# Performance work log

Hardware: AMD Instinct MI355X
Metric: run time of the kernel (lower is better)

The kernel has to match this reference:

```python
import jax, jax.numpy as jnp
import numpy as np

N = 50000   # nodes
E = 800000  # edges
IN = 64     # in_channels
ED = 16     # edge_dim
H = 4       # heads
C = 64      # per-head out channels (gnn_hidden_neurons)
G = 2048    # number of graphs in batch
OUT = 1
SLOPE = 0.2


def setup_inputs() -> dict:
    key = jax.random.key(0)
    ks = jax.random.split(key, 20)
    s = lambda fan_in: 1.0 / np.sqrt(fan_in)
    inp = {
        "x": jax.random.normal(ks[0], (N, IN), dtype=jnp.float32),
        "edge_index": jax.random.randint(ks[1], (2, E), 0, N, dtype=jnp.int64),
        "batch": jnp.sort(jax.random.randint(ks[2], (N,), 0, G, dtype=jnp.int64)),
        "edge_attr": jax.random.normal(ks[3], (E, ED), dtype=jnp.float32),
        # GATv2Conv layer 1 (in=IN)
        "Wl1": jax.random.normal(ks[4], (IN, H * C), dtype=jnp.float32) * s(IN),
        "Wr1": jax.random.normal(ks[5], (IN, H * C), dtype=jnp.float32) * s(IN),
        "We1": jax.random.normal(ks[6], (ED, H * C), dtype=jnp.float32) * s(ED),
        "att1": jax.random.normal(ks[7], (H, C), dtype=jnp.float32) * s(C),
        "b1": jnp.zeros((H * C,), dtype=jnp.float32),
        # GATv2Conv layer 2 (in=H*C)
        "Wl2": jax.random.normal(ks[8], (H * C, H * C), dtype=jnp.float32) * s(H * C),
        "Wr2": jax.random.normal(ks[9], (H * C, H * C), dtype=jnp.float32) * s(H * C),
        "We2": jax.random.normal(ks[10], (ED, H * C), dtype=jnp.float32) * s(ED),
        "att2": jax.random.normal(ks[11], (H, C), dtype=jnp.float32) * s(C),
        "b2": jnp.zeros((H * C,), dtype=jnp.float32),
        # FFN: Linear(H*C, OUT)
        "Wf": jax.random.normal(ks[12], (H * C, OUT), dtype=jnp.float32) * s(H * C),
        "bf": jnp.zeros((OUT,), dtype=jnp.float32),
    }
    return inp


def gatv2_layer(x, src, dst, ea, Wl, Wr, We, att, b):
    # x: [N, F], src/dst: [E2], ea: [E2, ED] (self-loops already included)
    n = x.shape[0]
    e2 = src.shape[0]
    xl = (x @ Wl).reshape(n, H, C)          # source transform
    xr = (x @ Wr).reshape(n, H, C)          # target transform
    ee = (ea @ We).reshape(e2, H, C)        # edge transform
    e = xl[src] + xr[dst] + ee              # [E2, H, C]
    e = jnp.where(e > 0, e, SLOPE * e)      # leaky_relu(0.2)
    score = jnp.einsum('ehc,hc->eh', e, att)
    # segment softmax over incoming edges of each destination node
    m = jax.ops.segment_max(score, dst, num_segments=n)
    m = jnp.where(jnp.isfinite(m), m, 0.0)
    ex = jnp.exp(score - m[dst])
    denom = jax.ops.segment_sum(ex, dst, num_segments=n)
    alpha = ex / (denom[dst] + 1e-16)       # [E2, H]
    out = jax.ops.segment_sum(alpha[:, :, None] * xl[src], dst, num_segments=n)
    return out.reshape(n, H * C) + b


def reference(x, edge_index, batch, edge_attr,
              Wl1, Wr1, We1, att1, b1,
              Wl2, Wr2, We2, att2, b2,
              Wf, bf):
    src, dst = edge_index[0], edge_index[1]
    # add self loops with fill_value='mean' edge attr (PyG GATv2Conv default)
    loop = jnp.arange(N, dtype=src.dtype)
    src2 = jnp.concatenate([src, loop])
    dst2 = jnp.concatenate([dst, loop])
    mean_ea = jnp.mean(edge_attr, axis=0)
    ea2 = jnp.concatenate([edge_attr, jnp.broadcast_to(mean_ea, (N, ED))], axis=0)

    h = gatv2_layer(x, src2, dst2, ea2, Wl1, Wr1, We1, att1, b1)
    h = jax.nn.relu(h)                      # activation (dropout = identity at eval)
    h = gatv2_layer(h, src2, dst2, ea2, Wl2, Wr2, We2, att2, b2)
    h = jax.nn.relu(h)

    # global mean pooling over graphs
    counts = jax.ops.segment_sum(jnp.ones((N,), dtype=h.dtype), batch, num_segments=G)
    pooled = jax.ops.segment_sum(h, batch, num_segments=G) / jnp.maximum(counts, 1.0)[:, None]

    # ffn_nlayers == 1: Dropout (identity) + Linear
    return pooled @ Wf + bf
```

## Files before the change

kernel.cpp:

```cpp
#include <hip/hip_runtime.h>
#include <math.h>

#define NN 50000
#define NE 800000
#define NE2 (NE + NN)
#define INC 64
#define EDD 16
#define NH 4
#define CC 64
#define HC 256
#define NG 2048
#define SLOPE 0.2f

typedef float v2f __attribute__((ext_vector_type(2)));
typedef float v4f __attribute__((ext_vector_type(4)));

#define RFL(x) __builtin_amdgcn_readfirstlane(x)

template <int CTRL, int RM>
__device__ __forceinline__ float dpp_add(float x) {
  int t = __builtin_amdgcn_update_dpp(0, __builtin_bit_cast(int, x),
                                      CTRL, RM, 0xF, false);
  return x + __builtin_bit_cast(float, t);
}
__device__ __forceinline__ float wave_sum_bcast(float x) {
  x = dpp_add<0x111, 0xF>(x);
  x = dpp_add<0x112, 0xF>(x);
  x = dpp_add<0x114, 0xF>(x);
  x = dpp_add<0x118, 0xF>(x);
  x = dpp_add<0x142, 0xA>(x);
  x = dpp_add<0x143, 0xC>(x);
  return __builtin_bit_cast(float,
      __builtin_amdgcn_readlane(__builtin_bit_cast(int, x), 63));
}

__global__ void ea_sum_kernel(const float* __restrict__ ea, float* __restrict__ meansum) {
  __shared__ float part[16];
  if (threadIdx.x < 16) part[threadIdx.x] = 0.f;
  __syncthreads();
  size_t stride = (size_t)gridDim.x * blockDim.x;
  size_t i = (size_t)blockIdx.x * blockDim.x + threadIdx.x;
  int cls = (int)(i & 15);
  float s = 0.f;
  const size_t total = (size_t)NE * EDD;
  for (; i < total; i += stride) s += ea[i];
  atomicAdd(&part[cls], s);
  __syncthreads();
  if (threadIdx.x < 16) atomicAdd(&meansum[threadIdx.x], part[threadIdx.x]);
}

__global__ void count_dst_kernel(const int* __restrict__ ei, int* __restrict__ counts) {
  int e = blockIdx.x * blockDim.x + threadIdx.x;
  if (e >= NE2) return;
  int d = (e < NE) ? ei[NE + e] : (e - NE);
  atomicAdd(&counts[d], 1);
}

__global__ void scan_partial_kernel(const int* __restrict__ counts, int n,
                                    int* __restrict__ excl, int* __restrict__ btot) {
  int b = blockIdx.x;
  int i = b * 256 + threadIdx.x;
  int v = (i < n) ? counts[i] : 0;
  int lane = threadIdx.x & 63;
  int incl = v;
#pragma unroll
  for (int off = 1; off < 64; off <<= 1) {
    int t = __shfl_up(incl, off, 64);
    if (lane >= off) incl += t;
  }
  __shared__ int wtot[4];
  int w = threadIdx.x >> 6;
  if (lane == 63) wtot[w] = incl;
  __syncthreads();
  int woff = 0;
#pragma unroll
  for (int k = 0; k < 4; ++k) woff += (k < w) ? wtot[k] : 0;
  incl += woff;
  if (i < n) excl[i] = incl - v;
  if (threadIdx.x == 255) btot[b] = incl;
}

__global__ void scan_btot_kernel(int* __restrict__ btot, int nb, int* __restrict__ totp,
                                 const float* __restrict__ meansum,
                                 float* __restrict__ meanea) {
  __shared__ int buf[256];
  int v = (threadIdx.x < nb) ? btot[threadIdx.x] : 0;
  buf[threadIdx.x] = v;
  __syncthreads();
  for (int off = 1; off < 256; off <<= 1) {
    int t = (threadIdx.x >= off) ? buf[threadIdx.x - off] : 0;
    __syncthreads();
    buf[threadIdx.x] += t;
    __syncthreads();
  }
  if (threadIdx.x < nb) btot[threadIdx.x] = buf[threadIdx.x] - v;
  if (threadIdx.x == 0) *totp = buf[nb - 1];
  if (threadIdx.x < 16) meanea[threadIdx.x] = meansum[threadIdx.x] * (1.0f / NE);
}

__global__ void scan_add_kernel(int* __restrict__ excl, int n, const int* __restrict__ btot,
                                const int* __restrict__ batch, int* __restrict__ gstart) {
  int i = blockIdx.x * 256 + threadIdx.x;
  if (i < n) excl[i] += btot[blockIdx.x];
  if (i < NN) {
    int b = batch[i];
    int prev = (i == 0) ? -1 : batch[i - 1];
    for (int g = prev + 1; g <= b; ++g) gstart[g] = i;
    if (i == NN - 1)
      for (int g = b + 1; g <= NG; ++g) gstart[g] = NN;
  }
}

__global__ void fill_kernel(const int* __restrict__ ei, const int* __restrict__ row_ptr,
                            int* __restrict__ cursor, int2* __restrict__ edg) {
  int e = blockIdx.x * blockDim.x + threadIdx.x;
  if (e >= NE2) return;
  int d, s;
  if (e < NE) { d = ei[NE + e]; s = ei[e]; }
  else        { d = e - NE;     s = d;     }
  int pos = row_ptr[d] + atomicAdd(&cursor[d], 1);
  edg[pos] = make_int2(e, s);
}

__global__ __launch_bounds__(256, 2) void gemm2_kernel(
    const float* __restrict__ X,
    const float* __restrict__ Wl, const float* __restrict__ Wr,
    float* __restrict__ Yl, float* __restrict__ Yr, int n, int K) {
  __shared__ float Xs[16][128];
  __shared__ float Ws[16][128];
  const int tid = threadIdx.x;
  const int row0 = blockIdx.x * 128;
  const int quad = blockIdx.y;
  const float* W = (quad < 2) ? Wl : Wr;
  float* Y = (quad < 2) ? Yl : Yr;
  const int col0 = (quad & 1) * 128;
  const int tr = tid >> 4, tc = tid & 15;
  float acc[8][8] = {};
  for (int k0 = 0; k0 < K; k0 += 16) {
    {
      int m = tid >> 1;
      int kq = (tid & 1) * 8;
      float4 v0 = make_float4(0.f, 0.f, 0.f, 0.f);
      float4 v1 = make_float4(0.f, 0.f, 0.f, 0.f);
      int r = row0 + m;
      if (r < n) {
        v0 = *(const float4*)(X + (size_t)r * K + k0 + kq);
        v1 = *(const float4*)(X + (size_t)r * K + k0 + kq + 4);
      }
      Xs[kq + 0][m] = v0.x; Xs[kq + 1][m] = v0.y;
      Xs[kq + 2][m] = v0.z; Xs[kq + 3][m] = v0.w;
      Xs[kq + 4][m] = v1.x; Xs[kq + 5][m] = v1.y;
      Xs[kq + 6][m] = v1.z; Xs[kq + 7][m] = v1.w;
    }
    {
      int kk = tid >> 4;
      int nq = (tid & 15) * 8;
      float4 w0 = *(const float4*)(W + (size_t)(k0 + kk) * HC + col0 + nq);
      float4 w1 = *(const float4*)(W + (size_t)(k0 + kk) * HC + col0 + nq + 4);
      *(float4*)(&Ws[kk][nq])     = w0;
      *(float4*)(&Ws[kk][nq + 4]) = w1;
    }
    __syncthreads();
#pragma unroll
    for (int k = 0; k < 16; ++k) {
      float a[8], b[8];
      *(float4*)(a)     = *(const float4*)(&Xs[k][tr * 8]);
      *(float4*)(a + 4) = *(const float4*)(&Xs[k][tr * 8 + 4]);
      *(float4*)(b)     = *(const float4*)(&Ws[k][tc * 8]);
      *(float4*)(b + 4) = *(const float4*)(&Ws[k][tc * 8 + 4]);
#pragma unroll
      for (int i = 0; i < 8; ++i)
#pragma unroll
        for (int jj = 0; jj < 8; ++jj) acc[i][jj] += a[i] * b[jj];
    }
    __syncthreads();
  }
#pragma unroll
  for (int i = 0; i < 8; ++i) {
    int r = row0 + tr * 8 + i;
    if (r < n) {
      *(float4*)(Y + (size_t)r * HC + col0 + tc * 8) =
          make_float4(acc[i][0], acc[i][1], acc[i][2], acc[i][3]);
      *(float4*)(Y + (size_t)r * HC + col0 + tc * 8 + 4) =
          make_float4(acc[i][4], acc[i][5], acc[i][6], acc[i][7]);
    }
  }
}

template <int B>
__device__ __forceinline__ void edge_batch(
    int j, const int2* __restrict__ edg, const float* __restrict__ xl,
    const float* __restrict__ ea, const v2f (&wreg)[8],
    float see, float xrl, float attl, unsigned c,
    float& den, float& acc) {
  int2 E[B];
#pragma unroll
  for (int k = 0; k < B; ++k) E[k] = edg[(unsigned)(j + k)];
  float X[B];
#pragma unroll
  for (int k = 0; k < B; ++k) X[k] = xl[((unsigned)E[k].y << 8) + c];
  float q[B];
#pragma unroll
  for (int k = 0; k < B; ++k) {
    float ee;
    if (E[k].x < NE) {
      const float* eap = ea + ((size_t)((unsigned)E[k].x << 4));
      v4f a0 = *(const v4f*)(eap);
      v4f a1 = *(const v4f*)(eap + 4);
      v4f a2 = *(const v4f*)(eap + 8);
      v4f a3 = *(const v4f*)(eap + 12);
      v2f s = (v2f){a0.x, a0.y} * wreg[0] + (v2f){a0.z, a0.w} * wreg[1]
            + (v2f){a1.x, a1.y} * wreg[2] + (v2f){a1.z, a1.w} * wreg[3]
            + (v2f){a2.x, a2.y} * wreg[4] + (v2f){a2.z, a2.w} * wreg[5]
            + (v2f){a3.x, a3.y} * wreg[6] + (v2f){a3.z, a3.w} * wreg[7];
      ee = s.x + s.y;
    } else {
      ee = see;
    }
    float t = X[k] + xrl + ee;
    t = fmaxf(t, SLOPE * t);
    q[k] = t * attl;
  }
#pragma unroll
  for (int k = 0; k < B; ++k) q[k] = wave_sum_bcast(q[k]);
#pragma unroll
  for (int k = 0; k < B; ++k) {
    float w = __builtin_amdgcn_exp2f(q[k]);
    den += w;
    acc = fmaf(w, X[k], acc);
  }
}

__global__ __launch_bounds__(256, 4) void edge_agg_kernel(
    const float* __restrict__ xl, const float* __restrict__ xr,
    const int* __restrict__ row_ptr, const int2* __restrict__ edg,
    const float* __restrict__ ea, const float* __restrict__ meanea,
    const float* __restrict__ We, const float* __restrict__ att,
    const float* __restrict__ bias, float* __restrict__ out) {
  const int lane = threadIdx.x & 63;
  const int head = threadIdx.x >> 6;
  const int node = blockIdx.x;
  const unsigned c = (unsigned)head * CC + (unsigned)lane;

  v2f wreg[8];
#pragma unroll
  for (int d = 0; d < 8; ++d)
    wreg[d] = (v2f){We[(unsigned)(2 * d) * HC + c], We[(unsigned)(2 * d + 1) * HC + c]};
  const float attl = att[c] * 1.44269504088896340736f;
  const float xrl  = xr[((unsigned)node << 8) + c];
  v2f seev = {0.f, 0.f};
#pragma unroll
  for (int d = 0; d < 8; ++d)
    seev += (v2f){meanea[2 * d], meanea[2 * d + 1]} * wreg[d];
  const float see = seev.x + seev.y;

  float den = 0.f, acc = 0.f;
  const int beg = row_ptr[node];
  const int end = row_ptr[node + 1];

  int j = beg;
  for (; j + 8 <= end; j += 8)
    edge_batch<8>(j, edg, xl, ea, wreg, see, xrl, attl, c, den, acc);
  const int rem = end - j;
  if (rem & 4) {
    edge_batch<4>(j, edg, xl, ea, wreg, see, xrl, attl, c, den, acc);
    j += 4;
  }
  if (rem & 2) {
    edge_batch<2>(j, edg, xl, ea, wreg, see, xrl, attl, c, den, acc);
    j += 2;
  }
  if (rem & 1) {
    edge_batch<1>(j, edg, xl, ea, wreg, see, xrl, attl, c, den, acc);
  }

  float o = fmaxf(acc / (den + 1e-16f) + bias[c], 0.f);
  out[((unsigned)node << 8) + c] = o;
}

__global__ void pool_kernel(const float* __restrict__ h2, const int* __restrict__ gstart,
                            float* __restrict__ pooled) {
  int lane = threadIdx.x & 63;
  int g = blockIdx.x * 4 + (threadIdx.x >> 6);
  if (g >= NG) return;
  int s = RFL(gstart[g]), e = RFL(gstart[g + 1]);
  float sx = 0.f, sy = 0.f, sz = 0.f, sw = 0.f;
  for (int i = s; i < e; ++i) {
    float4 v = *(const float4*)(h2 + (size_t)i * HC + lane * 4);
    sx += v.x; sy += v.y; sz += v.z; sw += v.w;
  }
  float inv = 1.f / fmaxf((float)(e - s), 1.f);
  *(float4*)(pooled + (size_t)g * HC + lane * 4) =
      make_float4(sx * inv, sy * inv, sz * inv, sw * inv);
}

__global__ void final_kernel(const float* __restrict__ pooled,
                             const float* __restrict__ Wf, const float* __restrict__ bf,
                             float* __restrict__ out) {
  int lane = threadIdx.x & 63;
  int g = blockIdx.x * (blockDim.x >> 6) + (threadIdx.x >> 6);
  if (g >= NG) return;
  float4 p = *(const float4*)(pooled + (size_t)g * HC + lane * 4);
  float4 w = *(const float4*)(Wf + lane * 4);
  float s = p.x * w.x + p.y * w.y + p.z * w.z + p.w * w.w;
  s += __shfl_xor(s, 1, 64);  s += __shfl_xor(s, 2, 64);
  s += __shfl_xor(s, 4, 64);  s += __shfl_xor(s, 8, 64);
  s += __shfl_xor(s, 16, 64); s += __shfl_xor(s, 32, 64);
  if (lane == 0) out[g] = s + bf[0];
}

extern "C" void kernel_launch(void* const* d_in, const int* in_sizes, int n_in,
                              void* d_out, int out_size, void* d_ws, size_t ws_size,
                              hipStream_t stream) {
  const float* x    = (const float*)d_in[0];
  const int*   ei   = (const int*)d_in[1];
  const int*   batch= (const int*)d_in[2];
  const float* ea   = (const float*)d_in[3];
  const float* Wl1  = (const float*)d_in[4];
  const float* Wr1  = (const float*)d_in[5];
  const float* We1  = (const float*)d_in[6];
  const float* att1 = (const float*)d_in[7];
  const float* b1   = (const float*)d_in[8];
  const float* Wl2  = (const float*)d_in[9];
  const float* Wr2  = (const float*)d_in[10];
  const float* We2  = (const float*)d_in[11];
  const float* att2 = (const float*)d_in[12];
  const float* b2   = (const float*)d_in[13];
  const float* Wf   = (const float*)d_in[14];
  const float* bf   = (const float*)d_in[15];
  float* out = (float*)d_out;

  float* xl      = (float*)d_ws;
  float* xr      = xl + (size_t)NN * HC;
  float* h1      = xr + (size_t)NN * HC;
  float* pooled  = h1 + (size_t)NN * HC;
  float* meansum = pooled + (size_t)NG * HC;
  float* meanea  = meansum + 16;
  int* counts  = (int*)(meanea + 16);
  int* row_ptr = counts + NN;
  int* btot    = row_ptr + NN + 1;
  int* gstart  = btot + 256;
  int2* edg    = (int2*)(gstart + NG + 1);

  const int NB = (NN + 255) / 256;

  hipMemsetAsync(counts, 0, NN * sizeof(int), stream);
  hipMemsetAsync(meansum, 0, 16 * sizeof(float), stream);

  ea_sum_kernel<<<1024, 256, 0, stream>>>(ea, meansum);

  count_dst_kernel<<<(NE2 + 255) / 256, 256, 0, stream>>>(ei, counts);
  scan_partial_kernel<<<NB, 256, 0, stream>>>(counts, NN, row_ptr, btot);
  scan_btot_kernel<<<1, 256, 0, stream>>>(btot, NB, row_ptr + NN, meansum, meanea);
  scan_add_kernel<<<NB, 256, 0, stream>>>(row_ptr, NN, btot, batch, gstart);
  hipMemsetAsync(counts, 0, NN * sizeof(int), stream);
  fill_kernel<<<(NE2 + 255) / 256, 256, 0, stream>>>(ei, row_ptr, counts, edg);

  dim3 ggrid((NN + 127) / 128, 4);
  gemm2_kernel<<<ggrid, 256, 0, stream>>>(x, Wl1, Wr1, xl, xr, NN, INC);
  edge_agg_kernel<<<NN, 256, 0, stream>>>(xl, xr, row_ptr, edg, ea, meanea,
                                          We1, att1, b1, h1);
  gemm2_kernel<<<ggrid, 256, 0, stream>>>(h1, Wl2, Wr2, xl, xr, NN, HC);
  edge_agg_kernel<<<NN, 256, 0, stream>>>(xl, xr, row_ptr, edg, ea, meanea,
                                          We2, att2, b2, h1);
  pool_kernel<<<(NG + 3) / 4, 256, 0, stream>>>(h1, gstart, pooled);
  final_kernel<<<(NG + 3) / 4, 256, 0, stream>>>(pooled, Wf, bf, out);
}
```

Baseline: 873.4 us.

## Replace FP32 SIMT GEMMs with split-bf16 MFMA GEMMs (3-pass hi/lo)

Replaces the FP32 FMA GEMM for the node transforms with a bf16 MFMA kernel that splits operands into hi and lo bf16 parts and accumulates hi*hi + hi*lo + lo*hi to approximate FP32 accuracy. Weights are split and transposed, and the layer-1 edge aggregation now writes its output directly as hi/lo bf16 so the second GEMM can consume it without a separate conversion pass. This adds several small split kernels, extra workspace, and three MFMA passes per GEMM. The new path runs only if the workspace is large enough, otherwise the old path is used.

```diff
diff --git a/kernel.cpp b/kernel.cpp
--- a/kernel.cpp
+++ b/kernel.cpp
@@ -14,8 +14,20 @@
 
 typedef float v2f __attribute__((ext_vector_type(2)));
 typedef float v4f __attribute__((ext_vector_type(4)));
+typedef __bf16 bf16x8 __attribute__((ext_vector_type(8)));
+typedef float f32x4 __attribute__((ext_vector_type(4)));
+typedef unsigned short ushort8v __attribute__((ext_vector_type(8)));
 
 #define RFL(x) __builtin_amdgcn_readfirstlane(x)
+
+__device__ __forceinline__ unsigned short f2bf(float f) {
+  unsigned u = __builtin_bit_cast(unsigned, f);
+  u += 0x7FFF + ((u >> 16) & 1);
+  return (unsigned short)(u >> 16);
+}
+__device__ __forceinline__ float bf2f(unsigned short h) {
+  return __builtin_bit_cast(float, ((unsigned)h) << 16);
+}
 
 template <int CTRL, int RM>
 __device__ __forceinline__ float dpp_add(float x) {
@@ -120,6 +132,100 @@
   else        { d = e - NE;     s = d;     }
   int pos = row_ptr[d] + atomicAdd(&cursor[d], 1);
   edg[pos] = make_int2(e, s);
+}
+
+__global__ void split4_kernel(const float* __restrict__ src, unsigned short* __restrict__ hi,
+                              unsigned short* __restrict__ lo, int total4) {
+  int i = blockIdx.x * blockDim.x + threadIdx.x;
+  if (i >= total4) return;
+  float4 v = ((const float4*)src)[i];
+  ushort4 h, l;
+  h.x = f2bf(v.x); l.x = f2bf(v.x - bf2f(h.x));
+  h.y = f2bf(v.y); l.y = f2bf(v.y - bf2f(h.y));
+  h.z = f2bf(v.z); l.z = f2bf(v.z - bf2f(h.z));
+  h.w = f2bf(v.w); l.w = f2bf(v.w - bf2f(h.w));
+  ((ushort4*)hi)[i] = h;
+  ((ushort4*)lo)[i] = l;
+}
+
+__global__ void split_wt_kernel(const float* __restrict__ W, int K,
+                                unsigned short* __restrict__ hi,
+                                unsigned short* __restrict__ lo) {
+  int idx = blockIdx.x * blockDim.x + threadIdx.x;
+  if (idx >= K * HC) return;
+  int k = idx >> 8, c = idx & 255;
+  float v = W[idx];
+  unsigned short h = f2bf(v);
+  hi[c * K + k] = h;
+  lo[c * K + k] = f2bf(v - bf2f(h));
+}
+
+__global__ __launch_bounds__(256, 2) void gemm_mfma_kernel(
+    const unsigned short* __restrict__ Ahi, const unsigned short* __restrict__ Alo,
+    const unsigned short* __restrict__ Wlhi, const unsigned short* __restrict__ Wllo,
+    const unsigned short* __restrict__ Wrhi, const unsigned short* __restrict__ Wrlo,
+    float* __restrict__ Yl, float* __restrict__ Yr, int n, int K) {
+  __shared__ unsigned short As[128][40];
+  __shared__ unsigned short Bs[128][40];
+  const int t = threadIdx.x;
+  const int row0 = blockIdx.x * 128;
+  const int quad = blockIdx.y;
+  const unsigned short* Bhi = (quad < 2) ? Wlhi : Wrhi;
+  const unsigned short* Blo = (quad < 2) ? Wllo : Wrlo;
+  float* Y = (quad < 2) ? Yl : Yr;
+  const int colbase = (quad & 1) * 128;
+  const int l = t & 63, w = t >> 6;
+  const int mw = (w >> 1) * 64, nw = (w & 1) * 64;
+  const int lr = l & 15, lk = (l >> 4) * 8;
+  const int srow = t >> 1, scb = (t & 1) << 4;
+
+  f32x4 acc[4][4] = {};
+  for (int seg = 0; seg < 3; ++seg) {
+    const unsigned short* Aseg = (seg == 2) ? Alo : Ahi;
+    const unsigned short* Bseg = (seg == 1) ? Blo : Bhi;
+    for (int k0 = 0; k0 < K; k0 += 32) {
+      {
+        uint4 v0 = {0, 0, 0, 0}, v1 = {0, 0, 0, 0};
+        int r = row0 + srow;
+        if (r < n) {
+          const uint4* p = (const uint4*)(Aseg + (size_t)r * K + k0 + scb);
+          v0 = p[0]; v1 = p[1];
+        }
+        *(uint4*)(&As[srow][scb])     = v0;
+        *(uint4*)(&As[srow][scb + 8]) = v1;
+      }
+      {
+        const uint4* p = (const uint4*)(Bseg + (size_t)(colbase + srow) * K + k0 + scb);
+        *(uint4*)(&Bs[srow][scb])     = p[0];
+        *(uint4*)(&Bs[srow][scb + 8]) = p[1];
+      }
+      __syncthreads();
+      bf16x8 a[4], b[4];
+#pragma unroll
+      for (int i = 0; i < 4; ++i)
+        a[i] = __builtin_bit_cast(bf16x8, *(const ushort8v*)(&As[mw + i * 16 + lr][lk]));
+#pragma unroll
+      for (int j = 0; j < 4; ++j)
+        b[j] = __builtin_bit_cast(bf16x8, *(const ushort8v*)(&Bs[nw + j * 16 + lr][lk]));
+#pragma unroll
+      for (int i = 0; i < 4; ++i)
+#pragma unroll
+        for (int j = 0; j < 4; ++j)
+          acc[i][j] = __builtin_amdgcn_mfma_f32_16x16x32_bf16(a[i], b[j], acc[i][j], 0, 0, 0);
+      __syncthreads();
+    }
+  }
+#pragma unroll
+  for (int i = 0; i < 4; ++i)
+#pragma unroll
+    for (int j = 0; j < 4; ++j) {
+      int colg = colbase + nw + j * 16 + lr;
+#pragma unroll
+      for (int r = 0; r < 4; ++r) {
+        int row = row0 + mw + i * 16 + (l >> 4) * 4 + r;
+        if (row < n) Y[(size_t)row * HC + colg] = acc[i][j][r];
+      }
+    }
 }
 
 __global__ __launch_bounds__(256, 2) void gemm2_kernel(
@@ -236,7 +342,8 @@
     const int* __restrict__ row_ptr, const int2* __restrict__ edg,
     const float* __restrict__ ea, const float* __restrict__ meanea,
     const float* __restrict__ We, const float* __restrict__ att,
-    const float* __restrict__ bias, float* __restrict__ out) {
+    const float* __restrict__ bias, float* __restrict__ out,
+    unsigned short* __restrict__ outhi, unsigned short* __restrict__ outlo) {
   const int lane = threadIdx.x & 63;
   const int head = threadIdx.x >> 6;
   const int node = blockIdx.x;
@@ -275,7 +382,14 @@
   }
 
   float o = fmaxf(acc / (den + 1e-16f) + bias[c], 0.f);
-  out[((unsigned)node << 8) + c] = o;
+  unsigned idx = ((unsigned)node << 8) + c;
+  if (outhi) {
+    unsigned short h = f2bf(o);
+    outhi[idx] = h;
+    outlo[idx] = f2bf(o - bf2f(h));
+  } else {
+    out[idx] = o;
+  }
 }
 
 __global__ void pool_kernel(const float* __restrict__ h2, const int* __restrict__ gstart,
@@ -340,7 +454,21 @@
   int* row_ptr = counts + NN;
   int* btot    = row_ptr + NN + 1;
   int* gstart  = btot + 256;
-  int2* edg    = (int2*)(gstart + NG + 1);
+  int2* edg    = (int2*)(gstart + NG + 2);
+  unsigned short* Xhi  = (unsigned short*)(edg + NE2);
+  unsigned short* Xlo  = Xhi + (size_t)NN * INC;
+  unsigned short* Hhi  = Xlo + (size_t)NN * INC;
+  unsigned short* Hlo  = Hhi + (size_t)NN * HC;
+  unsigned short* Wlh1 = Hlo + (size_t)NN * HC;
+  unsigned short* Wll1 = Wlh1 + HC * INC;
+  unsigned short* Wrh1 = Wll1 + HC * INC;
+  unsigned short* Wrl1 = Wrh1 + HC * INC;
+  unsigned short* Wlh2 = Wrl1 + HC * INC;
+  unsigned short* Wll2 = Wlh2 + HC * HC;
+  unsigned short* Wrh2 = Wll2 + HC * HC;
+  unsigned short* Wrl2 = Wrh2 + HC * HC;
+  size_t need = (size_t)((char*)(Wrl2 + HC * HC) - (char*)d_ws);
+  const bool use_mfma = (ws_size >= need);
 
   const int NB = (NN + 255) / 256;
 
@@ -356,13 +484,32 @@
   hipMemsetAsync(counts, 0, NN * sizeof(int), stream);
   fill_kernel<<<(NE2 + 255) / 256, 256, 0, stream>>>(ei, row_ptr, counts, edg);
 
-  dim3 ggrid((NN + 127) / 128, 4);
-  gemm2_kernel<<<ggrid, 256, 0, stream>>>(x, Wl1, Wr1, xl, xr, NN, INC);
-  edge_agg_kernel<<<NN, 256, 0, stream>>>(xl, xr, row_ptr, edg, ea, meanea,
-                                          We1, att1, b1, h1);
-  gemm2_kernel<<<ggrid, 256, 0, stream>>>(h1, Wl2, Wr2, xl, xr, NN, HC);
-  edge_agg_kernel<<<NN, 256, 0, stream>>>(xl, xr, row_ptr, edg, ea, meanea,
-                                          We2, att2, b2, h1);
+  if (use_mfma) {
+    split4_kernel<<<(NN * INC / 4 + 255) / 256, 256, 0, stream>>>(x, Xhi, Xlo, NN * INC / 4);
+    split_wt_kernel<<<(INC * HC + 255) / 256, 256, 0, stream>>>(Wl1, INC, Wlh1, Wll1);
+    split_wt_kernel<<<(INC * HC + 255) / 256, 256, 0, stream>>>(Wr1, INC, Wrh1, Wrl1);
+    split_wt_kernel<<<(HC * HC + 255) / 256, 256, 0, stream>>>(Wl2, HC, Wlh2, Wll2);
+    split_wt_kernel<<<(HC * HC + 255) / 256, 256, 0, stream>>>(Wr2, HC, Wrh2, Wrl2);
+
+    dim3 mgrid((NN + 127) / 128, 4);
+    gemm_mfma_kernel<<<mgrid, 256, 0, stream>>>(Xhi, Xlo, Wlh1, Wll1, Wrh1, Wrl1,
+                                                xl, xr, NN, INC);
+    edge_agg_kernel<<<NN, 256, 0, stream>>>(xl, xr, row_ptr, edg, ea, meanea,
+                                            We1, att1, b1, nullptr, Hhi, Hlo);
+    gemm_mfma_kernel<<<mgrid, 256, 0, stream>>>(Hhi, Hlo, Wlh2, Wll2, Wrh2, Wrl2,
+                                                xl, xr, NN, HC);
+    edge_agg_kernel<<<NN, 256, 0, stream>>>(xl, xr, row_ptr, edg, ea, meanea,
+                                            We2, att2, b2, h1, nullptr, nullptr);
+  } else {
+    dim3 ggrid((NN + 127) / 128, 4);
+    gemm2_kernel<<<ggrid, 256, 0, stream>>>(x, Wl1, Wr1, xl, xr, NN, INC);
+    edge_agg_kernel<<<NN, 256, 0, stream>>>(xl, xr, row_ptr, edg, ea, meanea,
+                                            We1, att1, b1, h1, nullptr, nullptr);
+    gemm2_kernel<<<ggrid, 256, 0, stream>>>(h1, Wl2, Wr2, xl, xr, NN, HC);
+    edge_agg_kernel<<<NN, 256, 0, stream>>>(xl, xr, row_ptr, edg, ea, meanea,
+                                            We2, att2, b2, h1, nullptr, nullptr);
+  }
+
   pool_kernel<<<(NG + 3) / 4, 256, 0, stream>>>(h1, gstart, pooled);
   final_kernel<<<(NG + 3) / 4, 256, 0, stream>>>(pooled, Wf, bf, out);
 }
```

New measurement: 815.8 us. -6.6%, faster.
